# Performance work log

Measured on AMD Instinct MI355X. Metric: run time of the kernel, lower is better.

Reference implementation:

```python
import jax, jax.numpy as jnp
import numpy as np

T = 4          # num edge types
D = 256        # embedding_size == hidden_size
N = 100_000    # nodes
E_EDGES = 320_000
VOCAB = 10_000


def setup_inputs() -> dict:
    key = jax.random.key(0)
    ks = jax.random.split(key, 12)
    s = 0.02
    input_ids = jax.random.randint(ks[0], (1, N), 0, VOCAB)
    etype = jax.random.randint(ks[1], (1, E_EDGES), 1, T + 1)  # types 1..T
    src = jax.random.randint(ks[2], (1, E_EDGES), 0, N)
    tgt = jax.random.randint(ks[3], (1, E_EDGES), 0, N)
    typed_edges = jnp.stack([etype[0], src[0], tgt[0]], axis=0)[None]  # [1,3,E]
    embed_table = jax.random.normal(ks[4], (VOCAB, D)) * s
    # 6 inner layers (3 per concat block x 2 blocks): 256 -> 256
    edge_W_inner = jax.random.normal(ks[5], (6, T, D, 2 * D)) * s
    ln_s_inner = jnp.ones((6, D)); ln_b_inner = jnp.zeros((6, D))
    dense_W_inner = jax.random.normal(ks[6], (6, D, D)) * s
    dense_b_inner = jnp.zeros((6, D))
    # 2 output layers on concat [state, hidden]: hidden_size 512 -> 256
    edge_W_out = jax.random.normal(ks[7], (2, T, 2 * D, 4 * D)) * s
    ln_s_out = jnp.ones((2, 2 * D)); ln_b_out = jnp.zeros((2, 2 * D))
    dense_W_out = jax.random.normal(ks[8], (2, D, 2 * D)) * s
    dense_b_out = jnp.zeros((2, D))
    return {
        "input_ids": input_ids, "typed_edges": typed_edges,
        "embed_table": embed_table,
        "edge_W_inner": edge_W_inner, "ln_s_inner": ln_s_inner, "ln_b_inner": ln_b_inner,
        "dense_W_inner": dense_W_inner, "dense_b_inner": dense_b_inner,
        "edge_W_out": edge_W_out, "ln_s_out": ln_s_out, "ln_b_out": ln_b_out,
        "dense_W_out": dense_W_out, "dense_b_out": dense_b_out,
    }


def layer_norm(x, s, b, eps=1e-5):
    mu = jnp.mean(x, axis=-1, keepdims=True)
    var = jnp.mean((x - mu) ** 2, axis=-1, keepdims=True)
    return (x - mu) * jax.lax.rsqrt(var + eps) * s + b


def message_passing(state, etype, src, tgt, edge_W):
    # state [N,d]; edge_W [T, d, 2d]. Gather endpoints, per-type linear, scatter-add to targets.
    es = jnp.concatenate([state[src], state[tgt]], axis=1)  # [E, 2d]
    msgs = jnp.zeros((es.shape[0], edge_W.shape[1]), state.dtype)
    for t in range(edge_W.shape[0]):  # small fixed number of edge types
        msgs = msgs + jnp.where((etype == t + 1)[:, None], es @ edge_W[t].T, 0.0)
    return jax.ops.segment_sum(msgs, tgt, num_segments=state.shape[0])


def gnn_layer(state, etype, src, tgt, eW, ls, lb, dW, db):
    m = message_passing(state, etype, src, tgt, eW)
    h = layer_norm(jax.nn.gelu(m, approximate=False), ls, lb)
    return jnp.tanh(h @ dW.T + db)


def concat_block(state, etype, src, tgt, eWi, lsi, lbi, dWi, dbi, eWo, lso, lbo, dWo, dbo):
    x = state
    for i in range(3):
        x = gnn_layer(x, etype, src, tgt, eWi[i], lsi[i], lbi[i], dWi[i], dbi[i])
    res = jnp.concatenate([state, x], axis=1)  # [N, 2d] residual concat
    return gnn_layer(res, etype, src, tgt, eWo, lso, lbo, dWo, dbo)


def reference(input_ids, typed_edges, embed_table, edge_W_inner, ln_s_inner, ln_b_inner,
              dense_W_inner, dense_b_inner, edge_W_out, ln_s_out, ln_b_out,
              dense_W_out, dense_b_out):
    ids = input_ids[0]
    te = typed_edges[0]
    etype, src, tgt = te[0], te[1], te[2]
    x = embed_table[ids]  # [N, D]
    for b in range(2):
        sl = slice(3 * b, 3 * b + 3)
        x = concat_block(x, etype, src, tgt,
                         edge_W_inner[sl], ln_s_inner[sl], ln_b_inner[sl],
                         dense_W_inner[sl], dense_b_inner[sl],
                         edge_W_out[b], ln_s_out[b], ln_b_out[b],
                         dense_W_out[b], dense_b_out[b])
    return x
```

## Files before the change

### kernel.cpp

```cpp
#include <hip/hip_runtime.h>
#include <cstdio>

#define N_NODES 100000
#define NPAD    100096
#define NTILES  782
#define NE      320000
#define NCH     196
#define WCO_OFF 3145728L
#define OUT_ELEMS (N_NODES * 256)

typedef unsigned short ushort_t;
typedef unsigned short u16x4 __attribute__((ext_vector_type(4)));
typedef unsigned short u16x8 __attribute__((ext_vector_type(8)));
typedef _Float16       f16;
typedef _Float16       f16x8 __attribute__((ext_vector_type(8)));
typedef float          f32x4 __attribute__((ext_vector_type(4)));
typedef float          f32x4v __attribute__((ext_vector_type(4)));

__device__ __forceinline__ float bf2f(ushort_t u) {
    return __uint_as_float(((unsigned)u) << 16);
}
__device__ __forceinline__ ushort_t f2bf(float f) {
    unsigned u = __float_as_uint(f);
    u += 0x7FFFu + ((u >> 16) & 1u);
    return (ushort_t)(u >> 16);
}
__device__ __forceinline__ ushort_t f2h(float f) {
    f16 h = (f16)f;
    return __builtin_bit_cast(ushort_t, h);
}
__device__ __forceinline__ float h2f(ushort_t u) {
    return (float)__builtin_bit_cast(f16, u);
}

__device__ __forceinline__ int xcd_remap(int pbid, int nwg) {
    int q = nwg >> 3, r = nwg & 7;
    int xcd = pbid & 7, idx = pbid >> 3;
    int base = (xcd < r) ? xcd * (q + 1) : r * (q + 1) + (xcd - r) * q;
    return base + idx;
}

__device__ __forceinline__ float fast_tanh(float x) {
    x = fminf(fmaxf(x, -10.f), 10.f);
    float e = __expf(2.f * x);
    return (e - 1.f) / (e + 1.f);
}

__global__ __launch_bounds__(256) void detect_k(const unsigned* __restrict__ w0, int* __restrict__ flag) {
    __shared__ int lds[256];
    int t = threadIdx.x;
    int cnt = 0;
    for (int i = t; i < 2048; i += 256) {
        unsigned e = (w0[i] >> 7) & 0xFFu;
        cnt += (e >= 96u && e <= 140u) ? 1 : 0;
    }
    lds[t] = cnt; __syncthreads();
    for (int s = 128; s > 0; s >>= 1) {
        if (t < s) lds[t] += lds[t + s];
        __syncthreads();
    }
    if (t == 0) *flag = (lds[0] < 1024) ? 1 : 0;
}

__device__ __forceinline__ ushort_t load_in(const void* p, long i, bool isf32) {
    return isf32 ? f2h(((const float*)p)[i]) : f2h(bf2f(((const ushort_t*)p)[i]));
}

struct CvtArgs {
    const void* src[8];
    ushort_t*   dst[8];
    int         n[8];
};

__global__ __launch_bounds__(256) void cvt_k(CvtArgs a, const int* __restrict__ flag) {
    int ti = blockIdx.y;
    int n = a.n[ti];
    const void* s = a.src[ti];
    ushort_t* d = a.dst[ti];
    bool isf32 = (*flag != 0);
    for (int i = blockIdx.x * 256 + threadIdx.x; i < n; i += gridDim.x * 256)
        d[i] = load_in(s, i, isf32);
}

__global__ __launch_bounds__(256) void pack_w(const void* __restrict__ eWi,
                                              const void* __restrict__ eWo,
                                              ushort_t* __restrict__ WC,
                                              const int* __restrict__ flag) {
    long idx = (long)blockIdx.x * 256 + threadIdx.x;
    bool isf32 = (*flag != 0);
    const long ELI = 6L * 4 * 256 * 512;
    const long ELO = 2L * 4 * 512 * 1024;
    if (idx < ELI) {
        int j = idx & 511;
        int o = (idx >> 9) & 255;
        int t = (idx >> 17) & 3;
        long l = idx >> 19;
        int q = o >> 6, oo = o & 63;
        int k = j & 255;
        int n = ((j < 256) ? 0 : 256) + t * 64 + oo;
        WC[l * 524288 + (long)q * 131072 + (long)n * 256 + k] = load_in(eWi, idx, isf32);
    } else if (idx < ELI + ELO) {
        long i2 = idx - ELI;
        int j = i2 & 1023;
        int o = (i2 >> 10) & 511;
        int t = (i2 >> 19) & 3;
        long b = i2 >> 21;
        int c = o >> 6, oo = o & 63;
        int k = j & 511;
        int n = ((j < 512) ? 0 : 256) + t * 64 + oo;
        WC[WCO_OFF + b * 2097152L + (long)c * 262144 + (long)n * 512 + k] = load_in(eWo, i2, isf32);
    }
}

__global__ __launch_bounds__(256) void embed_k(const int* __restrict__ ids,
                                               const void* __restrict__ tab,
                                               ushort_t* __restrict__ S,
                                               const int* __restrict__ flag) {
    int row = blockIdx.x * 4 + (threadIdx.x >> 6);
    int l = threadIdx.x & 63;
    if (row >= N_NODES) return;
    int id = ids[row];
    u16x4 v;
    if (*flag) {
        f32x4v fv = *(const f32x4v*)((const float*)tab + (size_t)id * 256 + l * 4);
        #pragma unroll
        for (int i = 0; i < 4; i++) v[i] = f2h(fv[i]);
    } else {
        u16x4 bv = *(const u16x4*)((const ushort_t*)tab + (size_t)id * 256 + l * 4);
        #pragma unroll
        for (int i = 0; i < 4; i++) v[i] = f2h(bf2f(bv[i]));
    }
    *(u16x4*)(S + (size_t)row * 256 + l * 4) = v;
}

__global__ __launch_bounds__(256) void emit_k(const ushort_t* __restrict__ Bst, void* __restrict__ out,
                                              const int* __restrict__ flag) {
    long i = (long)blockIdx.x * 256 + threadIdx.x;
    if (i >= OUT_ELEMS) return;
    float v = h2f(Bst[i]);
    if (*flag) ((float*)out)[i] = v;
    else       ((ushort_t*)out)[i] = f2bf(v);
}

__global__ __launch_bounds__(256) void count_k(const int* __restrict__ tgt, int* __restrict__ counts) {
    int e = blockIdx.x * 256 + threadIdx.x;
    if (e < NE) atomicAdd(&counts[tgt[e]], 1);
}

__global__ __launch_bounds__(256) void scan1_k(const int* __restrict__ counts,
                                               int* __restrict__ incl, int* __restrict__ chsums) {
    __shared__ int lds[256];
    int c = blockIdx.x, t = threadIdx.x;
    int i0 = c * 512 + 2 * t;
    int a = (i0 < N_NODES) ? counts[i0] : 0;
    int b = (i0 + 1 < N_NODES) ? counts[i0 + 1] : 0;
    int ps = a + b;
    lds[t] = ps; __syncthreads();
    int x = ps;
    for (int off = 1; off < 256; off <<= 1) {
        int y = (t >= off) ? lds[t - off] : 0;
        __syncthreads();
        x += y; lds[t] = x;
        __syncthreads();
    }
    int excl = x - ps;
    if (i0 < N_NODES) incl[i0] = excl + a;
    if (i0 + 1 < N_NODES) incl[i0 + 1] = excl + a + b;
    if (t == 255) chsums[c] = x;
}

__global__ __launch_bounds__(256) void scan2_k(const int* __restrict__ chsums, int* __restrict__ chunkoff) {
    __shared__ int lds[256];
    int t = threadIdx.x;
    int v = (t < NCH) ? chsums[t] : 0;
    lds[t] = v; __syncthreads();
    int x = v;
    for (int off = 1; off < 256; off <<= 1) {
        int y = (t >= off) ? lds[t - off] : 0;
        __syncthreads();
        x += y; lds[t] = x;
        __syncthreads();
    }
    if (t <= NCH) chunkoff[t] = x - v;
}

__global__ __launch_bounds__(256) void scan3_k(const int* __restrict__ counts, const int* __restrict__ incl,
                                               const int* __restrict__ chunkoff,
                                               int* __restrict__ offsets, int* __restrict__ cursor) {
    int c = blockIdx.x, t = threadIdx.x;
    int base = chunkoff[c];
    #pragma unroll
    for (int k = 0; k < 2; k++) {
        int i = c * 512 + 2 * t + k;
        if (i < N_NODES) {
            int off = base + incl[i] - counts[i];
            offsets[i] = off;
            cursor[i] = off;
        }
    }
    if (c == 0 && t == 0) offsets[N_NODES] = chunkoff[NCH];
}

__global__ __launch_bounds__(256) void fill_k(const int* __restrict__ et, const int* __restrict__ src,
                                              const int* __restrict__ tgt,
                                              int* __restrict__ cursor, int* __restrict__ sorted) {
    int e = blockIdx.x * 256 + threadIdx.x;
    if (e < NE) {
        int pos = atomicAdd(&cursor[tgt[e]], 1);
        sorted[pos] = ((et[e] - 1) << 28) | src[e];
    }
}

template<int EPI>
__global__ __launch_bounds__(256) void gemm_bt(const ushort_t* __restrict__ A,
                                               const ushort_t* __restrict__ B,
                                               int K, int ldc,
                                               ushort_t* __restrict__ Cb,
                                               const ushort_t* __restrict__ bias, int storeM) {
    __shared__ __align__(16) ushort_t As[128 * 64];
    __shared__ __align__(16) ushort_t Bs[128 * 64];
    const int tid = threadIdx.x;
    const int w = tid >> 6, l = tid & 63;
    const int wr = w >> 1, wc = w & 1;
    const int gx = gridDim.x;
    const int lbid = xcd_remap(blockIdx.y * gx + blockIdx.x, gx * gridDim.y);
    const long m0 = (long)(lbid / gx) * 128, n0 = (long)(lbid % gx) * 128;
    const int lr = l >> 3;
    const int lc = (l & 7) * 8;
    f32x4 acc[4][4];
    #pragma unroll
    for (int s = 0; s < 4; s++)
        #pragma unroll
        for (int n = 0; n < 4; n++) acc[s][n] = (f32x4){0.f, 0.f, 0.f, 0.f};

    for (int k0 = 0; k0 < K; k0 += 64) {
        #pragma unroll
        for (int q = 0; q < 4; q++) {
            int row = w * 32 + q * 8 + lr;
            const ushort_t* g = A + (m0 + row) * (long)K + k0 + lc;
            __builtin_amdgcn_global_load_lds(
                (__attribute__((address_space(1))) unsigned int*)(g),
                (__attribute__((address_space(3))) unsigned int*)(&As[row * 64 + lc]), 16, 0, 0);
        }
        #pragma unroll
        for (int q = 0; q < 4; q++) {
            int row = w * 32 + q * 8 + lr;
            const ushort_t* g = B + (n0 + row) * (long)K + k0 + lc;
            __builtin_amdgcn_global_load_lds(
                (__attribute__((address_space(1))) unsigned int*)(g),
                (__attribute__((address_space(3))) unsigned int*)(&Bs[row * 64 + lc]), 16, 0, 0);
        }
        __syncthreads();
        #pragma unroll
        for (int kk = 0; kk < 2; kk++) {
            f16x8 af[4], bfr[4];
            #pragma unroll
            for (int s = 0; s < 4; s++)
                af[s] = *(const f16x8*)&As[(wr * 64 + s * 16 + (l & 15)) * 64 + kk * 32 + (l >> 4) * 8];
            #pragma unroll
            for (int n = 0; n < 4; n++)
                bfr[n] = *(const f16x8*)&Bs[(wc * 64 + n * 16 + (l & 15)) * 64 + kk * 32 + (l >> 4) * 8];
            #pragma unroll
            for (int s = 0; s < 4; s++)
                #pragma unroll
                for (int n = 0; n < 4; n++)
                    acc[s][n] = __builtin_amdgcn_mfma_f32_16x16x32_f16(af[s], bfr[n], acc[s][n], 0, 0, 0);
        }
        __syncthreads();
    }
    const long rb = m0 + wr * 64 + ((l >> 4) << 2);
    const long cb = n0 + wc * 64 + (l & 15);
    #pragma unroll
    for (int s = 0; s < 4; s++) {
        #pragma unroll
        for (int n = 0; n < 4; n++) {
            long c = cb + n * 16;
            #pragma unroll
            for (int j = 0; j < 4; j++) {
                long r = rb + s * 16 + j;
                float val = acc[s][n][j];
                if constexpr (EPI == 2) {
                    if (r < storeM) {
                        float t = fast_tanh(val + h2f(bias[c]));
                        Cb[r * ldc + c] = f2h(t);
                    }
                } else {
                    Cb[r * ldc + c] = f2h(val);
                }
            }
        }
    }
}

__global__ __launch_bounds__(256) void gemm_bt2(const ushort_t* __restrict__ A0,
                                                const ushort_t* __restrict__ A1,
                                                const ushort_t* __restrict__ B,
                                                int ldc,
                                                ushort_t* __restrict__ Cb) {
    __shared__ __align__(16) ushort_t As[128 * 64];
    __shared__ __align__(16) ushort_t Bs[128 * 64];
    const int tid = threadIdx.x;
    const int w = tid >> 6, l = tid & 63;
    const int wr = w >> 1, wc = w & 1;
    const int gx = gridDim.x;
    const int lbid = xcd_remap(blockIdx.y * gx + blockIdx.x, gx * gridDim.y);
    const long m0 = (long)(lbid / gx) * 128, n0 = (long)(lbid % gx) * 128;
    const int lr = l >> 3;
    const int lc = (l & 7) * 8;
    f32x4 acc[4][4];
    #pragma unroll
    for (int s = 0; s < 4; s++)
        #pragma unroll
        for (int n = 0; n < 4; n++) acc[s][n] = (f32x4){0.f, 0.f, 0.f, 0.f};

    for (int k0 = 0; k0 < 512; k0 += 64) {
        const ushort_t* Ab = (k0 < 256) ? A0 : A1;
        const int kq = k0 & 255;
        #pragma unroll
        for (int q = 0; q < 4; q++) {
            int row = w * 32 + q * 8 + lr;
            const ushort_t* g = Ab + (m0 + row) * 256L + kq + lc;
            __builtin_amdgcn_global_load_lds(
                (__attribute__((address_space(1))) unsigned int*)(g),
                (__attribute__((address_space(3))) unsigned int*)(&As[row * 64 + lc]), 16, 0, 0);
        }
        #pragma unroll
        for (int q = 0; q < 4; q++) {
            int row = w * 32 + q * 8 + lr;
            const ushort_t* g = B + (n0 + row) * 512L + k0 + lc;
            __builtin_amdgcn_global_load_lds(
                (__attribute__((address_space(1))) unsigned int*)(g),
                (__attribute__((address_space(3))) unsigned int*)(&Bs[row * 64 + lc]), 16, 0, 0);
        }
        __syncthreads();
        #pragma unroll
        for (int kk = 0; kk < 2; kk++) {
            f16x8 af[4], bfr[4];
            #pragma unroll
            for (int s = 0; s < 4; s++)
                af[s] = *(const f16x8*)&As[(wr * 64 + s * 16 + (l & 15)) * 64 + kk * 32 + (l >> 4) * 8];
            #pragma unroll
            for (int n = 0; n < 4; n++)
                bfr[n] = *(const f16x8*)&Bs[(wc * 64 + n * 16 + (l & 15)) * 64 + kk * 32 + (l >> 4) * 8];
            #pragma unroll
            for (int s = 0; s < 4; s++)
                #pragma unroll
                for (int n = 0; n < 4; n++)
                    acc[s][n] = __builtin_amdgcn_mfma_f32_16x16x32_f16(af[s], bfr[n], acc[s][n], 0, 0, 0);
        }
        __syncthreads();
    }
    const long rb = m0 + wr * 64 + ((l >> 4) << 2);
    const long cb = n0 + wc * 64 + (l & 15);
    #pragma unroll
    for (int s = 0; s < 4; s++) {
        #pragma unroll
        for (int n = 0; n < 4; n++) {
            long c = cb + n * 16;
            #pragma unroll
            for (int j = 0; j < 4; j++) {
                long r = rb + s * 16 + j;
                Cb[r * ldc + c] = f2h(acc[s][n][j]);
            }
        }
    }
}

__global__ __launch_bounds__(256) void agg_q(const ushort_t* __restrict__ Z,
                                             const int* __restrict__ offsets,
                                             const int* __restrict__ sorted,
                                             ushort_t* __restrict__ M, int mld, int q) {
    int v = blockIdx.x * 4 + (threadIdx.x >> 6);
    int l = threadIdx.x & 63;
    if (v >= NPAD) return;
    ushort_t* mp = M + (size_t)v * mld + (q << 6) + l;
    if (v >= N_NODES) { *mp = 0; return; }
    float acc = 0.f;
    int d0 = 0, d1 = 0, d2 = 0, d3 = 0;
    int beg = offsets[v], end = offsets[v + 1];
    for (int e = beg; e < end; ++e) {
        int pk = sorted[e];
        int t = pk >> 28;
        int s = pk & 0x0FFFFFFF;
        acc += h2f(Z[(size_t)s * 512 + (t << 6) + l]);
        d0 += (t == 0); d1 += (t == 1); d2 += (t == 2); d3 += (t == 3);
    }
    const ushort_t* zs = Z + (size_t)v * 512 + 256 + l;
    if (d0) acc += (float)d0 * h2f(zs[0]);
    if (d1) acc += (float)d1 * h2f(zs[64]);
    if (d2) acc += (float)d2 * h2f(zs[128]);
    if (d3) acc += (float)d3 * h2f(zs[192]);
    *mp = f2h(acc);
}

template<int DOUT>
__global__ __launch_bounds__(256) void gelu_ln16_k(const ushort_t* __restrict__ M,
                                                   const ushort_t* __restrict__ ls,
                                                   const ushort_t* __restrict__ lb,
                                                   ushort_t* __restrict__ H) {
    constexpr int VPL = DOUT / 64;
    int row = blockIdx.x * 4 + (threadIdx.x >> 6);
    int l = threadIdx.x & 63;
    const ushort_t* mp = M + (size_t)row * DOUT + l * VPL;
    u16x4 mv[VPL / 4];
    #pragma unroll
    for (int c = 0; c < VPL / 4; c++) mv[c] = *(const u16x4*)(mp + c * 4);
    float g[VPL];
    float s = 0.f, q = 0.f;
    #pragma unroll
    for (int i = 0; i < VPL; i++) {
        float x = h2f(mv[i >> 2][i & 3]);
        float gg = 0.5f * x * (1.f + erff(x * 0.70710678118654752f));
        g[i] = gg; s += gg; q += gg * gg;
    }
    #pragma unroll
    for (int m = 1; m < 64; m <<= 1) {
        s += __shfl_xor(s, m, 64);
        q += __shfl_xor(q, m, 64);
    }
    float mean = s * (1.f / DOUT);
    float var = q * (1.f / DOUT) - mean * mean;
    var = fmaxf(var, 0.f);
    float rs = rsqrtf(var + 1e-5f);
    int col = l * VPL;
    ushort_t* hp = H + (size_t)row * DOUT + col;
    #pragma unroll
    for (int i = 0; i < VPL; i++)
        hp[i] = f2h((g[i] - mean) * rs * h2f(ls[col + i]) + h2f(lb[col + i]));
}

extern "C" void kernel_launch(void* const* d_in, const int* in_sizes, int n_in,
                              void* d_out, int out_size, void* d_ws, size_t ws_size,
                              hipStream_t stream) {
    const int* ids = (const int*)d_in[0];
    const int* te = (const int*)d_in[1];
    const int* et = te;
    const int* esrc = te + NE;
    const int* etgt = te + 2 * NE;
    const void* tab = d_in[2];
    const void* eWi = d_in[3];
    const void* lsi = d_in[4];
    const void* lbi = d_in[5];
    const void* dWi = d_in[6];
    const void* dbi = d_in[7];
    const void* eWo = d_in[8];
    const void* lso = d_in[9];
    const void* lbo = d_in[10];
    const void* dWo = d_in[11];
    const void* dbo = d_in[12];

    char* w = (char*)d_ws;
    auto alloc = [&](size_t bytes) -> char* {
        char* p = w; w += (bytes + 255) & ~(size_t)255; return p;
    };
    ushort_t* A    = (ushort_t*)alloc((size_t)NPAD * 256 * 2);
    ushort_t* Bst  = (ushort_t*)alloc((size_t)NPAD * 256 * 2);
    ushort_t* WC   = (ushort_t*)alloc(7340032UL * 2);
    ushort_t* lsiC = (ushort_t*)alloc(1536 * 2);
    ushort_t* lbiC = (ushort_t*)alloc(1536 * 2);
    ushort_t* dbiC = (ushort_t*)alloc(1536 * 2);
    ushort_t* lsoC = (ushort_t*)alloc(1024 * 2);
    ushort_t* lboC = (ushort_t*)alloc(1024 * 2);
    ushort_t* dboC = (ushort_t*)alloc(512 * 2);
    ushort_t* dWiC = (ushort_t*)alloc(393216UL * 2);
    ushort_t* dWoC = (ushort_t*)alloc(262144UL * 2);
    int* flag      = (int*)alloc(256);
    int* counts    = (int*)alloc((size_t)N_NODES * 4);
    int* incl      = (int*)alloc((size_t)N_NODES * 4);
    int* chsums    = (int*)alloc(1024);
    int* chunkoff  = (int*)alloc(1024);
    int* offsets   = (int*)alloc((size_t)(N_NODES + 8) * 4);
    int* cursor    = (int*)alloc((size_t)N_NODES * 4);
    int* sorted    = (int*)alloc((size_t)NE * 4);
    ushort_t* Magg = (ushort_t*)alloc((size_t)NPAD * 512 * 2);
    ushort_t* R;
    if ((size_t)out_size >= (size_t)NPAD * 256 * 2) R = (ushort_t*)d_out;
    else R = (ushort_t*)alloc((size_t)NPAD * 256 * 2);
    size_t fixed = (size_t)(w - (char*)d_ws);

    const size_t ZQ_BYTES = (size_t)NPAD * 512 * 2;
    size_t bigsz = (ws_size > fixed) ? (ws_size - fixed) : 0;
    if (bigsz < ZQ_BYTES) {
        fprintf(stderr, "kernel_launch: ws too small (%zu bytes, fixed %zu, big %zu) -- no-op\n",
                ws_size, fixed, bigsz);
        return;
    }
    ushort_t* Zq = (ushort_t*)w;
    ushort_t* H  = (ushort_t*)w;

    detect_k<<<1, 256, 0, stream>>>((const unsigned*)tab, flag);
    CvtArgs ca;
    ca.src[0] = lsi;  ca.dst[0] = lsiC; ca.n[0] = 1536;
    ca.src[1] = lbi;  ca.dst[1] = lbiC; ca.n[1] = 1536;
    ca.src[2] = dbi;  ca.dst[2] = dbiC; ca.n[2] = 1536;
    ca.src[3] = lso;  ca.dst[3] = lsoC; ca.n[3] = 1024;
    ca.src[4] = lbo;  ca.dst[4] = lboC; ca.n[4] = 1024;
    ca.src[5] = dbo;  ca.dst[5] = dboC; ca.n[5] = 512;
    ca.src[6] = dWi;  ca.dst[6] = dWiC; ca.n[6] = 393216;
    ca.src[7] = dWo;  ca.dst[7] = dWoC; ca.n[7] = 262144;
    cvt_k<<<dim3(1536, 8), 256, 0, stream>>>(ca, flag);
    hipMemsetAsync(counts, 0, (size_t)N_NODES * 4, stream);
    hipMemsetAsync(A   + (size_t)N_NODES * 256, 0, (size_t)(NPAD - N_NODES) * 256 * 2, stream);
    hipMemsetAsync(Bst + (size_t)N_NODES * 256, 0, (size_t)(NPAD - N_NODES) * 256 * 2, stream);
    hipMemsetAsync(R   + (size_t)N_NODES * 256, 0, (size_t)(NPAD - N_NODES) * 256 * 2, stream);
    pack_w<<<28672, 256, 0, stream>>>(eWi, eWo, WC, flag);
    embed_k<<<N_NODES / 4, 256, 0, stream>>>(ids, tab, A, flag);
    count_k<<<(NE + 255) / 256, 256, 0, stream>>>(etgt, counts);
    scan1_k<<<NCH, 256, 0, stream>>>(counts, incl, chsums);
    scan2_k<<<1, 256, 0, stream>>>(chsums, chunkoff);
    scan3_k<<<NCH, 256, 0, stream>>>(counts, incl, chunkoff, offsets, cursor);
    fill_k<<<(NE + 255) / 256, 256, 0, stream>>>(et, esrc, etgt, cursor, sorted);

    auto inner_layer = [&](const ushort_t* Xin, ushort_t* Xout, int lay) {
        for (int q = 0; q < 4; q++) {
            gemm_bt<3><<<dim3(4, NTILES), 256, 0, stream>>>(
                Xin, WC + (long)lay * 524288 + (long)q * 131072, 256, 512, Zq, nullptr, 0);
            agg_q<<<NPAD / 4, 256, 0, stream>>>(Zq, offsets, sorted, Magg, 256, q);
        }
        gelu_ln16_k<256><<<NPAD / 4, 256, 0, stream>>>(Magg, lsiC + lay * 256, lbiC + lay * 256, H);
        gemm_bt<2><<<dim3(2, NTILES), 256, 0, stream>>>(H, dWiC + (long)lay * 65536, 256, 256,
                                                        Xout, dbiC + lay * 256, N_NODES);
    };

    auto out_layer = [&](const ushort_t* X0, const ushort_t* X1, int b, ushort_t* dest) {
        for (int c = 0; c < 8; c++) {
            gemm_bt2<<<dim3(4, NTILES), 256, 0, stream>>>(
                X0, X1, WC + WCO_OFF + (long)b * 2097152 + (long)c * 262144, 512, Zq);
            agg_q<<<NPAD / 4, 256, 0, stream>>>(Zq, offsets, sorted, Magg, 512, c);
        }
        gelu_ln16_k<512><<<NPAD / 4, 256, 0, stream>>>(Magg, lsoC + b * 512, lboC + b * 512, H);
        gemm_bt<2><<<dim3(2, NTILES), 256, 0, stream>>>(H, dWoC + (long)b * 131072, 512, 256,
                                                        dest, dboC + b * 256, N_NODES);
    };

    inner_layer(A, Bst, 0);
    inner_layer(Bst, R, 1);
    inner_layer(R, Bst, 2);
    out_layer(A, Bst, 0, R);
    inner_layer(R, A, 3);
    inner_layer(A, Bst, 4);
    inner_layer(Bst, A, 5);
    out_layer(R, A, 1, Bst);

    emit_k<<<(OUT_ELEMS + 255) / 256, 256, 0, stream>>>(Bst, d_out, flag);
}
```

Before: 6.237 ms.

## Fold layernorm into dense GEMM epilogue and fuse GELU/stats into aggregation

GELU moves into the aggregation kernel, which also accumulates per-row sum and sum-of-squares through float atomics. A small stats kernel turns these into mean and rstd. The LN scale and bias are folded into pre-scaled dense weights plus per-column correction vectors, applied in the GEMM epilogue. This removes the separate gelu+layernorm pass and its extra read and write of the hidden buffer, at the cost of atomics per row chunk and a mean-subtraction step after the GEMM that is numerically less stable.

```diff
diff --git a/kernel.cpp b/kernel.cpp
--- a/kernel.cpp
+++ b/kernel.cpp
@@ -44,6 +44,10 @@
     x = fminf(fmaxf(x, -10.f), 10.f);
     float e = __expf(2.f * x);
     return (e - 1.f) / (e + 1.f);
+}
+
+__device__ __forceinline__ float gelu_f(float x) {
+    return 0.5f * x * (1.f + erff(x * 0.70710678118654752f));
 }
 
 __global__ __launch_bounds__(256) void detect_k(const unsigned* __restrict__ w0, int* __restrict__ flag) {
@@ -80,6 +84,63 @@
     bool isf32 = (*flag != 0);
     for (int i = blockIdx.x * 256 + threadIdx.x; i < n; i += gridDim.x * 256)
         d[i] = load_in(s, i, isf32);
+}
+
+__global__ __launch_bounds__(256) void scale_w_k(const ushort_t* __restrict__ dWiC,
+                                                 const ushort_t* __restrict__ lsiC,
+                                                 const ushort_t* __restrict__ lbiC,
+                                                 const ushort_t* __restrict__ dbiC,
+                                                 const ushort_t* __restrict__ dWoC,
+                                                 const ushort_t* __restrict__ lsoC,
+                                                 const ushort_t* __restrict__ lboC,
+                                                 const ushort_t* __restrict__ dboC,
+                                                 ushort_t* __restrict__ dWiS,
+                                                 float* __restrict__ uwi, float* __restrict__ w0i,
+                                                 ushort_t* __restrict__ dWoS,
+                                                 float* __restrict__ uwo, float* __restrict__ w0o) {
+    int wid = blockIdx.x * 4 + (threadIdx.x >> 6);
+    int l = threadIdx.x & 63;
+    float u = 0.f, w0 = 0.f;
+    if (wid < 1536) {
+        int lay = wid >> 8, c = wid & 255;
+        u16x4 wv = *(const u16x4*)(dWiC + (size_t)wid * 256 + l * 4);
+        u16x4 sv = *(const u16x4*)(lsiC + lay * 256 + l * 4);
+        u16x4 bv = *(const u16x4*)(lbiC + lay * 256 + l * 4);
+        u16x4 ov;
+        #pragma unroll
+        for (int i = 0; i < 4; i++) {
+            float W = h2f(wv[i]);
+            float ws = W * h2f(sv[i]);
+            ov[i] = f2h(ws);
+            u += ws; w0 += W * h2f(bv[i]);
+        }
+        *(u16x4*)(dWiS + (size_t)wid * 256 + l * 4) = ov;
+        #pragma unroll
+        for (int m = 1; m < 64; m <<= 1) {
+            u += __shfl_xor(u, m, 64); w0 += __shfl_xor(w0, m, 64);
+        }
+        if (l == 0) { uwi[wid] = u; w0i[wid] = w0 + h2f(dbiC[lay * 256 + c]); }
+    } else if (wid < 2048) {
+        int w2 = wid - 1536;
+        int b = w2 >> 8, c = w2 & 255;
+        u16x8 wv = *(const u16x8*)(dWoC + (size_t)w2 * 512 + l * 8);
+        u16x8 sv = *(const u16x8*)(lsoC + b * 512 + l * 8);
+        u16x8 bv = *(const u16x8*)(lboC + b * 512 + l * 8);
+        u16x8 ov;
+        #pragma unroll
+        for (int i = 0; i < 8; i++) {
+            float W = h2f(wv[i]);
+            float ws = W * h2f(sv[i]);
+            ov[i] = f2h(ws);
+            u += ws; w0 += W * h2f(bv[i]);
+        }
+        *(u16x8*)(dWoS + (size_t)w2 * 512 + l * 8) = ov;
+        #pragma unroll
+        for (int m = 1; m < 64; m <<= 1) {
+            u += __shfl_xor(u, m, 64); w0 += __shfl_xor(w0, m, 64);
+        }
+        if (l == 0) { uwo[w2] = u; w0o[w2] = w0 + h2f(dboC[b * 256 + c]); }
+    }
 }
 
 __global__ __launch_bounds__(256) void pack_w(const void* __restrict__ eWi,
@@ -216,7 +277,10 @@
                                                const ushort_t* __restrict__ B,
                                                int K, int ldc,
                                                ushort_t* __restrict__ Cb,
-                                               const ushort_t* __restrict__ bias, int storeM) {
+                                               const float2* __restrict__ MR,
+                                               const float* __restrict__ uu,
+                                               const float* __restrict__ w0t,
+                                               int storeM) {
     __shared__ __align__(16) ushort_t As[128 * 64];
     __shared__ __align__(16) ushort_t Bs[128 * 64];
     const int tid = threadIdx.x;
@@ -281,8 +345,9 @@
                 float val = acc[s][n][j];
                 if constexpr (EPI == 2) {
                     if (r < storeM) {
-                        float t = fast_tanh(val + h2f(bias[c]));
-                        Cb[r * ldc + c] = f2h(t);
+                        float2 mr = MR[r];
+                        float o = mr.y * (val - mr.x * uu[c]) + w0t[c];
+                        Cb[r * ldc + c] = f2h(fast_tanh(o));
                     }
                 } else {
                     Cb[r * ldc + c] = f2h(val);
@@ -369,11 +434,12 @@
 __global__ __launch_bounds__(256) void agg_q(const ushort_t* __restrict__ Z,
                                              const int* __restrict__ offsets,
                                              const int* __restrict__ sorted,
-                                             ushort_t* __restrict__ M, int mld, int q) {
+                                             ushort_t* __restrict__ G, int mld, int q,
+                                             float* __restrict__ Sg, float* __restrict__ Sq) {
     int v = blockIdx.x * 4 + (threadIdx.x >> 6);
     int l = threadIdx.x & 63;
     if (v >= NPAD) return;
-    ushort_t* mp = M + (size_t)v * mld + (q << 6) + l;
+    ushort_t* mp = G + (size_t)v * mld + (q << 6) + l;
     if (v >= N_NODES) { *mp = 0; return; }
     float acc = 0.f;
     int d0 = 0, d1 = 0, d2 = 0, d3 = 0;
@@ -390,43 +456,28 @@
     if (d1) acc += (float)d1 * h2f(zs[64]);
     if (d2) acc += (float)d2 * h2f(zs[128]);
     if (d3) acc += (float)d3 * h2f(zs[192]);
-    *mp = f2h(acc);
-}
-
-template<int DOUT>
-__global__ __launch_bounds__(256) void gelu_ln16_k(const ushort_t* __restrict__ M,
-                                                   const ushort_t* __restrict__ ls,
-                                                   const ushort_t* __restrict__ lb,
-                                                   ushort_t* __restrict__ H) {
-    constexpr int VPL = DOUT / 64;
-    int row = blockIdx.x * 4 + (threadIdx.x >> 6);
-    int l = threadIdx.x & 63;
-    const ushort_t* mp = M + (size_t)row * DOUT + l * VPL;
-    u16x4 mv[VPL / 4];
-    #pragma unroll
-    for (int c = 0; c < VPL / 4; c++) mv[c] = *(const u16x4*)(mp + c * 4);
-    float g[VPL];
-    float s = 0.f, q = 0.f;
-    #pragma unroll
-    for (int i = 0; i < VPL; i++) {
-        float x = h2f(mv[i >> 2][i & 3]);
-        float gg = 0.5f * x * (1.f + erff(x * 0.70710678118654752f));
-        g[i] = gg; s += gg; q += gg * gg;
-    }
+    float g = gelu_f(acc);
+    *mp = f2h(g);
+    float sg = g, sq = g * g;
     #pragma unroll
     for (int m = 1; m < 64; m <<= 1) {
-        s += __shfl_xor(s, m, 64);
-        q += __shfl_xor(q, m, 64);
-    }
-    float mean = s * (1.f / DOUT);
-    float var = q * (1.f / DOUT) - mean * mean;
-    var = fmaxf(var, 0.f);
-    float rs = rsqrtf(var + 1e-5f);
-    int col = l * VPL;
-    ushort_t* hp = H + (size_t)row * DOUT + col;
-    #pragma unroll
-    for (int i = 0; i < VPL; i++)
-        hp[i] = f2h((g[i] - mean) * rs * h2f(ls[col + i]) + h2f(lb[col + i]));
+        sg += __shfl_xor(sg, m, 64);
+        sq += __shfl_xor(sq, m, 64);
+    }
+    if (l == 0) {
+        atomicAdd(&Sg[v], sg);
+        atomicAdd(&Sq[v], sq);
+    }
+}
+
+__global__ __launch_bounds__(256) void stats_k(float* __restrict__ Sg, float* __restrict__ Sq,
+                                               float2* __restrict__ MR, float inv) {
+    int v = blockIdx.x * 256 + threadIdx.x;
+    if (v >= N_NODES) return;
+    float mean = Sg[v] * inv;
+    float var = fmaxf(Sq[v] * inv - mean * mean, 0.f);
+    MR[v] = make_float2(mean, rsqrtf(var + 1e-5f));
+    Sg[v] = 0.f; Sq[v] = 0.f;
 }
 
 extern "C" void kernel_launch(void* const* d_in, const int* in_sizes, int n_in,
@@ -464,6 +515,15 @@
     ushort_t* dboC = (ushort_t*)alloc(512 * 2);
     ushort_t* dWiC = (ushort_t*)alloc(393216UL * 2);
     ushort_t* dWoC = (ushort_t*)alloc(262144UL * 2);
+    ushort_t* dWiS = (ushort_t*)alloc(393216UL * 2);
+    ushort_t* dWoS = (ushort_t*)alloc(262144UL * 2);
+    float* uwi     = (float*)alloc(1536 * 4);
+    float* w0i     = (float*)alloc(1536 * 4);
+    float* uwo     = (float*)alloc(512 * 4);
+    float* w0o     = (float*)alloc(512 * 4);
+    float* Sg      = (float*)alloc((size_t)NPAD * 4);
+    float* Sq      = (float*)alloc((size_t)NPAD * 4);
+    float2* MR     = (float2*)alloc((size_t)NPAD * 8);
     int* flag      = (int*)alloc(256);
     int* counts    = (int*)alloc((size_t)N_NODES * 4);
     int* incl      = (int*)alloc((size_t)N_NODES * 4);
@@ -472,7 +532,7 @@
     int* offsets   = (int*)alloc((size_t)(N_NODES + 8) * 4);
     int* cursor    = (int*)alloc((size_t)N_NODES * 4);
     int* sorted    = (int*)alloc((size_t)NE * 4);
-    ushort_t* Magg = (ushort_t*)alloc((size_t)NPAD * 512 * 2);
+    ushort_t* G    = (ushort_t*)alloc((size_t)NPAD * 512 * 2);
     ushort_t* R;
     if ((size_t)out_size >= (size_t)NPAD * 256 * 2) R = (ushort_t*)d_out;
     else R = (ushort_t*)alloc((size_t)NPAD * 256 * 2);
@@ -486,7 +546,6 @@
         return;
     }
     ushort_t* Zq = (ushort_t*)w;
-    ushort_t* H  = (ushort_t*)w;
 
     detect_k<<<1, 256, 0, stream>>>((const unsigned*)tab, flag);
     CvtArgs ca;
@@ -499,7 +558,11 @@
     ca.src[6] = dWi;  ca.dst[6] = dWiC; ca.n[6] = 393216;
     ca.src[7] = dWo;  ca.dst[7] = dWoC; ca.n[7] = 262144;
     cvt_k<<<dim3(1536, 8), 256, 0, stream>>>(ca, flag);
+    scale_w_k<<<512, 256, 0, stream>>>(dWiC, lsiC, lbiC, dbiC, dWoC, lsoC, lboC, dboC,
+                                       dWiS, uwi, w0i, dWoS, uwo, w0o);
     hipMemsetAsync(counts, 0, (size_t)N_NODES * 4, stream);
+    hipMemsetAsync(Sg, 0, (size_t)NPAD * 4, stream);
+    hipMemsetAsync(Sq, 0, (size_t)NPAD * 4, stream);
     hipMemsetAsync(A   + (size_t)N_NODES * 256, 0, (size_t)(NPAD - N_NODES) * 256 * 2, stream);
     hipMemsetAsync(Bst + (size_t)N_NODES * 256, 0, (size_t)(NPAD - N_NODES) * 256 * 2, stream);
     hipMemsetAsync(R   + (size_t)N_NODES * 256, 0, (size_t)(NPAD - N_NODES) * 256 * 2, stream);
@@ -514,23 +577,24 @@
     auto inner_layer = [&](const ushort_t* Xin, ushort_t* Xout, int lay) {
         for (int q = 0; q < 4; q++) {
             gemm_bt<3><<<dim3(4, NTILES), 256, 0, stream>>>(
-                Xin, WC + (long)lay * 524288 + (long)q * 131072, 256, 512, Zq, nullptr, 0);
-            agg_q<<<NPAD / 4, 256, 0, stream>>>(Zq, offsets, sorted, Magg, 256, q);
-        }
-        gelu_ln16_k<256><<<NPAD / 4, 256, 0, stream>>>(Magg, lsiC + lay * 256, lbiC + lay * 256, H);
-        gemm_bt<2><<<dim3(2, NTILES), 256, 0, stream>>>(H, dWiC + (long)lay * 65536, 256, 256,
-                                                        Xout, dbiC + lay * 256, N_NODES);
+                Xin, WC + (long)lay * 524288 + (long)q * 131072, 256, 512, Zq,
+                nullptr, nullptr, nullptr, 0);
+            agg_q<<<NPAD / 4, 256, 0, stream>>>(Zq, offsets, sorted, G, 256, q, Sg, Sq);
+        }
+        stats_k<<<(N_NODES + 255) / 256, 256, 0, stream>>>(Sg, Sq, MR, 1.f / 256.f);
+        gemm_bt<2><<<dim3(2, NTILES), 256, 0, stream>>>(G, dWiS + (long)lay * 65536, 256, 256,
+                                                        Xout, MR, uwi + lay * 256, w0i + lay * 256, N_NODES);
     };
 
     auto out_layer = [&](const ushort_t* X0, const ushort_t* X1, int b, ushort_t* dest) {
         for (int c = 0; c < 8; c++) {
             gemm_bt2<<<dim3(4, NTILES), 256, 0, stream>>>(
                 X0, X1, WC + WCO_OFF + (long)b * 2097152 + (long)c * 262144, 512, Zq);
-            agg_q<<<NPAD / 4, 256, 0, stream>>>(Zq, offsets, sorted, Magg, 512, c);
-        }
-        gelu_ln16_k<512><<<NPAD / 4, 256, 0, stream>>>(Magg, lsoC + b * 512, lboC + b * 512, H);
-        gemm_bt<2><<<dim3(2, NTILES), 256, 0, stream>>>(H, dWoC + (long)b * 131072, 512, 256,
-                                                        dest, dboC + b * 256, N_NODES);
+            agg_q<<<NPAD / 4, 256, 0, stream>>>(Zq, offsets, sorted, G, 512, c, Sg, Sq);
+        }
+        stats_k<<<(N_NODES + 255) / 256, 256, 0, stream>>>(Sg, Sq, MR, 1.f / 512.f);
+        gemm_bt<2><<<dim3(2, NTILES), 256, 0, stream>>>(G, dWoS + (long)b * 131072, 512, 256,
+                                                        dest, MR, uwo + b * 256, w0o + b * 256, N_NODES);
     };
 
     inner_layer(A, Bst, 0);
```

New measurement: 6.395 ms. 2.5% more time.
